# Performance work log

Measured on AMD Instinct MI355X. Metric: run time of the kernel, lower is better.

The kernel has to match this reference:

```python
import jax, jax.numpy as jnp
import numpy as np
import math

H = 512        # hidden_size (channels)
N = 64         # state_size
MAX_LEN = 4096 # kernel length L
BATCH = 8
SEQ = 4096     # seq len of input (== MAX_LEN here)


def _nplr(n):
    # HiPPO-LegS NPLR decomposition (done once at init, numpy float64 for eig stability)
    i = np.arange(n, dtype=np.float64)
    j = np.sqrt(2 * i + 1)
    A = -(np.tril(j[None, :] * j[:, None]) - np.diag(i))
    Bv = j.astype(np.complex128)
    p = j / np.sqrt(2.0)
    w, V = np.linalg.eig(A + p[None, :] * p[:, None])  # normal part; conj-pair eigvals adjacent
    w = w[::2].copy()          # [N/2]
    V = V[:, ::2].copy()       # [N, N/2]
    Bc = V.conj().T @ Bv       # [N/2]
    pc = V.conj().T @ p.astype(np.complex128)
    V_full = np.concatenate([V, V.conj()], axis=-1)      # [N, N]
    VtAV = V_full.conj().T @ A.astype(np.complex128) @ V_full  # [N, N]
    return w, pc, V, Bc, VtAV


def _ri(c):
    # complex -> trailing real/imag pair, float32 (mirrors torch.view_as_real)
    return np.stack([c.real, c.imag], axis=-1).astype(np.float32)


def setup_inputs() -> dict:
    rng = np.random.default_rng(0)
    w, p, V, Bc, Amat = _nplr(N)
    Brep = np.tile(Bc[None, :], (H, 1))                      # [H, N/2]
    C = rng.standard_normal((H, N)).astype(np.complex128)
    C = C @ V.conj()                                         # einsum('hn,nm->hm') -> [H, N/2]
    log_dt = math.log(1e-3) + (math.log(1e-1) - math.log(1e-3)) * rng.random(H)
    dt = np.exp(log_dt)[:, None, None]
    I = np.eye(N, dtype=np.complex128)[None]
    dA = np.linalg.inv(I - dt * Amat / 2) @ (I + dt * Amat / 2)   # [H, N, N]
    dA_power = I - np.linalg.matrix_power(dA, MAX_LEN)
    C2 = np.concatenate([C, C.conj()], axis=-1)              # [H, N]
    C2 = np.einsum('hmn,hm->hn', dA_power.conj(), C2)[:, : N // 2]
    p_rep = np.tile(p[None, None, :], (H, 1, 1))             # [H, 1, N/2]
    Bfull = np.concatenate([Brep[:, None, :], p_rep], axis=1)  # [H, 2, N/2]
    Cfull = np.concatenate([C2[:, None, :], p_rep], axis=1)    # [H, 2, N/2] (q == p)

    key = jax.random.key(0)
    kx, kd = jax.random.split(key)
    return {
        "x": jax.random.normal(kx, (BATCH, SEQ, H), dtype=jnp.float32),
        "log_dt": jnp.asarray(log_dt, dtype=jnp.float32),   # [H]
        "w_ri": jnp.asarray(_ri(w)),                        # [N/2, 2]
        "B_ri": jnp.asarray(_ri(Bfull)),                    # [H, 2, N/2, 2]
        "C_ri": jnp.asarray(_ri(Cfull)),                    # [H, 2, N/2, 2]
        "D": jax.random.normal(kd, (H,), dtype=jnp.float32),
    }


def _s4_kernel(log_dt, w_ri, B_ri, C_ri):
    L = MAX_LEN
    w = w_ri[..., 0] + 1j * w_ri[..., 1]   # [n] with n = N/2
    B = B_ri[..., 0] + 1j * B_ri[..., 1]   # [H, 2, n]
    C = C_ri[..., 0] + 1j * C_ri[..., 1]   # [H, 2, n]
    dt = jnp.exp(log_dt)                   # [H]
    freq = jnp.exp(-2j * jnp.pi / L * jnp.arange(L // 2 + 1))  # [F], F = L/2+1
    z = 2 * (1 - freq) / (1 + freq)        # bilinear-transformed frequencies

    v = C[:, :, None, :].conj() * B[:, None, :, :]   # [H, 2, 2, n]
    wd = w[None, :] * dt[:, None]                    # [H, n]
    # cauchy_mult: r = sum_n v/(z-w) + conj(v)/(z-conj(w)), as batched matmuls over n
    K1 = 1.0 / (z[None, None, :] - wd[:, :, None])          # [H, n, F]
    K2 = 1.0 / (z[None, None, :] - wd.conj()[:, :, None])   # [H, n, F]
    r = jnp.einsum('habn,hnf->habf', v, K1) + jnp.einsum('habn,hnf->habf', v.conj(), K2)
    r = r * dt[:, None, None, None]
    # Woodbury correction for the rank-1 (p, q) augmentation
    k_f = r[:, 0, 0, :] - r[:, 0, 1, :] * r[:, 1, 0, :] / (1 + r[:, 1, 1, :])  # [H, F]
    k_f = k_f * 2 / (1 + freq)
    return jnp.fft.irfft(k_f)   # [H, L]


def reference(x, log_dt, w_ri, B_ri, C_ri, D):
    k = _s4_kernel(log_dt, w_ri, B_ri, C_ri)     # [H, L]
    xt = jnp.transpose(x, (0, 2, 1))             # [B, H, Lx]
    L2 = 2 * MAX_LEN                              # conv pads to 2*kernel_len
    k_f = jnp.fft.rfft(k, n=L2)                  # [H, L2/2+1]
    x_f = jnp.fft.rfft(xt, n=L2)                 # [B, H, L2/2+1]
    y = jnp.fft.irfft(k_f[None] * x_f, n=L2)[..., : xt.shape[-1]]
    y = y + xt * D[None, :, None]                # skip connection
    return jnp.transpose(y, (0, 2, 1))           # [B, Lx, H]
```

## Files before the change

### kernel.cpp

```cpp
#include <hip/hip_runtime.h>
#include <math.h>

#define TPB 256
#define CTPB 512
#define KTPB 512

__device__ __forceinline__ float2 cmul(float2 a, float2 b) {
    return make_float2(a.x * b.x - a.y * b.y, a.x * b.y + a.y * b.x);
}
__device__ __forceinline__ float2 cdivf(float2 a, float2 b) {
    float inv = 1.0f / (b.x * b.x + b.y * b.y);
    return make_float2((a.x * b.x + a.y * b.y) * inv, (a.y * b.x - a.x * b.y) * inv);
}
__device__ __forceinline__ float2 cadd(float2 a, float2 b) { return make_float2(a.x + b.x, a.y + b.y); }
__device__ __forceinline__ float2 csub(float2 a, float2 b) { return make_float2(a.x - b.x, a.y - b.y); }
__device__ __forceinline__ float2 mul_i(float2 a, float d) {
    return make_float2(-d * a.y, d * a.x);
}
__device__ __forceinline__ int brev11(int x) { return (int)(__brev((unsigned)x) >> 21); }
__device__ __forceinline__ int rev8(int x) {
    return ((x & 7) << 9) | (((x >> 3) & 7) << 6) | (((x >> 6) & 7) << 3) | ((x >> 9) & 7);
}
__device__ __forceinline__ int swz(int i) { return i ^ ((i >> 4) & 15) ^ ((i >> 8) & 15); }

__device__ __forceinline__ void dft8(const float2* x, float2* y, float d) {
    const float r = 0.70710678118f;
    float2 s0 = cadd(x[0], x[4]), t0 = csub(x[0], x[4]);
    float2 s1 = cadd(x[1], x[5]), t1 = csub(x[1], x[5]);
    float2 s2 = cadd(x[2], x[6]), t2 = csub(x[2], x[6]);
    float2 s3 = cadd(x[3], x[7]), t3 = csub(x[3], x[7]);
    t1 = cmul(t1, make_float2(r, d * r));
    t2 = mul_i(t2, d);
    t3 = cmul(t3, make_float2(-r, d * r));
    float2 u0 = cadd(s0, s2), v0 = csub(s0, s2);
    float2 u1 = cadd(s1, s3), v1 = mul_i(csub(s1, s3), d);
    y[0] = cadd(u0, u1); y[4] = csub(u0, u1);
    y[2] = cadd(v0, v1); y[6] = csub(v0, v1);
    float2 p0 = cadd(t0, t2), q0 = csub(t0, t2);
    float2 p1 = cadd(t1, t3), q1 = mul_i(csub(t1, t3), d);
    y[1] = cadd(p0, p1); y[5] = csub(p0, p1);
    y[3] = cadd(q0, q1); y[7] = csub(q0, q1);
}

__device__ __forceinline__ void dft8z(float2 x0, float2 x1, float2 x2, float2 x3,
                                      float2* y, float d) {
    const float r = 0.70710678118f;
    float2 u0 = cadd(x0, x2), v0 = csub(x0, x2);
    float2 u1 = cadd(x1, x3), v1 = mul_i(csub(x1, x3), d);
    float2 t1 = cmul(x1, make_float2(r, d * r));
    float2 t2 = mul_i(x2, d);
    float2 t3 = cmul(x3, make_float2(-r, d * r));
    float2 p0 = cadd(x0, t2), q0 = csub(x0, t2);
    float2 p1 = cadd(t1, t3), q1 = mul_i(csub(t1, t3), d);
    y[0] = cadd(u0, u1); y[4] = csub(u0, u1);
    y[2] = cadd(v0, v1); y[6] = csub(v0, v1);
    y[1] = cadd(p0, p1); y[5] = csub(p0, p1);
    y[3] = cadd(q0, q1); y[7] = csub(q0, q1);
}

__device__ __forceinline__ void dft8_lo(const float2* x, float2* y, float d) {
    const float r = 0.70710678118f;
    float2 s0 = cadd(x[0], x[4]), t0 = csub(x[0], x[4]);
    float2 s1 = cadd(x[1], x[5]), t1 = csub(x[1], x[5]);
    float2 s2 = cadd(x[2], x[6]), t2 = csub(x[2], x[6]);
    float2 s3 = cadd(x[3], x[7]), t3 = csub(x[3], x[7]);
    t1 = cmul(t1, make_float2(r, d * r));
    t2 = mul_i(t2, d);
    t3 = cmul(t3, make_float2(-r, d * r));
    float2 u0 = cadd(s0, s2), v0 = csub(s0, s2);
    float2 u1 = cadd(s1, s3), v1 = mul_i(csub(s1, s3), d);
    y[0] = cadd(u0, u1);
    y[2] = cadd(v0, v1);
    float2 p0 = cadd(t0, t2), q0 = csub(t0, t2);
    float2 p1 = cadd(t1, t3), q1 = mul_i(csub(t1, t3), d);
    y[1] = cadd(p0, p1);
    y[3] = cadd(q0, q1);
}

template <int HB, int DIR>
__device__ __forceinline__ void dif_stage(float2* s, int tid) {
    __syncthreads();
    const int h = 1 << HB;
    int j = tid & (h - 1);
    int base = ((tid >> HB) << (HB + 3)) + j;
    int s0 = swz(base);
    float2 x[8];
#pragma unroll
    for (int k = 0; k < 8; ++k) x[k] = s[s0 ^ swz(k << HB)];
    float2 y[8];
    dft8(x, y, (float)DIR);
    if constexpr (HB != 0) {
        float ang = (float)DIR * 6.283185307179586f / (float)(h << 3) * (float)j;
        float c, sn;
        __sincosf(ang, &sn, &c);
        float2 w = make_float2(c, sn), wm = w;
        s[s0] = y[0];
#pragma unroll
        for (int m = 1; m < 8; ++m) {
            s[s0 ^ swz(m << HB)] = cmul(wm, y[m]);
            wm = cmul(wm, w);
        }
    } else {
#pragma unroll
        for (int m = 0; m < 8; ++m) s[s0 ^ swz(m << HB)] = y[m];
    }
}

template <int HB, int DIR>
__device__ __forceinline__ void dit_stage(float2* s, int tid) {
    __syncthreads();
    const int h = 1 << HB;
    int j = tid & (h - 1);
    int base = ((tid >> HB) << (HB + 3)) + j;
    int s0 = swz(base);
    float2 x[8];
    if constexpr (HB != 0) {
        float ang = (float)DIR * 6.283185307179586f / (float)(h << 3) * (float)j;
        float c, sn;
        __sincosf(ang, &sn, &c);
        float2 w = make_float2(c, sn);
        x[0] = s[s0];
        float2 wm = w;
#pragma unroll
        for (int k = 1; k < 8; ++k) {
            x[k] = cmul(wm, s[s0 ^ swz(k << HB)]);
            wm = cmul(wm, w);
        }
    } else {
#pragma unroll
        for (int k = 0; k < 8; ++k) x[k] = s[s0 ^ swz(k << HB)];
    }
    float2 y[8];
    dft8(x, y, (float)DIR);
#pragma unroll
    for (int m = 0; m < 8; ++m) s[s0 ^ swz(m << HB)] = y[m];
}

template <int LOGN, int NT>
__device__ void fft8_dif(float2* s, int tid, float dir) {
    const int N = 1 << LOGN;
#pragma unroll
    for (int hb = LOGN - 3; hb >= 0; hb -= 3) {
        const int h = 1 << hb;
        const float astep = dir * 6.283185307179586f / (float)(h << 3);
        __syncthreads();
#pragma unroll
        for (int it = 0; it < (N >> 3) / NT; ++it) {
            const int b = tid + it * NT;
            int j = b & (h - 1);
            int base = ((b >> hb) << (hb + 3)) + j;
            int s0 = swz(base);
            float2 x[8];
#pragma unroll
            for (int k = 0; k < 8; ++k) x[k] = s[s0 ^ swz(k << hb)];
            float2 y[8];
            dft8(x, y, dir);
            if (hb != 0) {
                float ang = astep * (float)j;
                float c, sn;
                __sincosf(ang, &sn, &c);
                float2 w = make_float2(c, sn), wm = w;
                s[s0] = y[0];
#pragma unroll
                for (int m = 1; m < 8; ++m) {
                    s[s0 ^ swz(m << hb)] = cmul(wm, y[m]);
                    wm = cmul(wm, w);
                }
            } else {
#pragma unroll
                for (int m = 0; m < 8; ++m) s[s0 ^ swz(m << hb)] = y[m];
            }
        }
    }
    __syncthreads();
}

template <int LOGN, int NT>
__device__ void fft_dif2(float2* s, int tid, float dir) {
    const int N = 1 << LOGN;
    for (int st = LOGN - 1; st >= 0; --st) {
        __syncthreads();
        int half = 1 << st;
        for (int b = tid; b < (N >> 1); b += NT) {
            int j  = b & (half - 1);
            int i0 = ((b >> st) << (st + 1)) + j;
            int i1 = i0 + half;
            float2 u = s[i0], v = s[i1];
            float2 d = make_float2(u.x - v.x, u.y - v.y);
            s[i0] = make_float2(u.x + v.x, u.y + v.y);
            if (half > 1) {
                float ang = dir * 3.14159265358979f * (float)j / (float)half;
                float c, sn;
                __sincosf(ang, &sn, &c);
                s[i1] = cmul(make_float2(c, sn), d);
            } else {
                s[i1] = d;
            }
        }
    }
    __syncthreads();
}

__global__ __launch_bounds__(TPB) void kf_kernel(
    const float* __restrict__ log_dt, const float* __restrict__ w_ri,
    const float* __restrict__ Bri, const float* __restrict__ Cri,
    float2* __restrict__ kf) {
    __shared__ float2 wds[32];
    __shared__ float aab[4][32], rab[4][32];
    __shared__ float qn[32], pn[32];
    const int h   = blockIdx.x;
    const int tid = threadIdx.x;
    const float dt = expf(log_dt[h]);
    if (tid < 32) {
        float wr = w_ri[2 * tid] * dt, wi = w_ri[2 * tid + 1] * dt;
        wds[tid] = make_float2(wr, wi);
        qn[tid]  = wr * wr + wi * wi;
        pn[tid]  = -2.0f * wr;
    }
    __syncthreads();
    if (tid < 128) {
        int a = tid >> 6, b = (tid >> 5) & 1, n = tid & 31;
        const float* Cp = Cri + (((h * 2 + a) * 32) + n) * 2;
        const float* Bp = Bri + (((h * 2 + b) * 32) + n) * 2;
        float Cr = Cp[0], Ci = Cp[1], Br = Bp[0], Bi = Bp[1];
        float2 v = make_float2(Cr * Br + Ci * Bi, Cr * Bi - Ci * Br);
        float2 wd = wds[n];
        aab[a * 2 + b][n] = -2.0f * (v.x * wd.x + v.y * wd.y);
        rab[a * 2 + b][n] = 2.0f * v.x;
    }
    __syncthreads();
    const int by   = blockIdx.y;
    const int fend = (by == 3) ? 2049 : (by + 1) * 512;
    for (int f = by * 512 + tid; f < fend; f += TPB) {
        float th = (6.283185307179586f / 4096.0f) * (float)f;
        float cf = cosf(th), sf = sinf(th);
        float2 den = make_float2(1.0f + cf, -sf);
        float zt  = 2.0f * tanf(0.5f * th);
        float zt2 = zt * zt;
        float2 r00 = make_float2(0.f, 0.f), r01 = r00, r10 = r00, r11 = r00;
        for (int n = 0; n < 32; ++n) {
            float c   = qn[n] - zt2;
            float d   = pn[n] * zt;
            float inv = 1.0f / (c * c + d * d);
            float cc = c * inv, dd = d * inv;
            float a0 = aab[0][n], b0 = rab[0][n] * zt;
            r00.x += a0 * cc + b0 * dd; r00.y += b0 * cc - a0 * dd;
            float a1 = aab[1][n], b1 = rab[1][n] * zt;
            r01.x += a1 * cc + b1 * dd; r01.y += b1 * cc - a1 * dd;
            float a2 = aab[2][n], b2 = rab[2][n] * zt;
            r10.x += a2 * cc + b2 * dd; r10.y += b2 * cc - a2 * dd;
            float a3 = aab[3][n], b3 = rab[3][n] * zt;
            r11.x += a3 * cc + b3 * dd; r11.y += b3 * cc - a3 * dd;
        }
        r00.x *= dt; r00.y *= dt; r01.x *= dt; r01.y *= dt;
        r10.x *= dt; r10.y *= dt; r11.x *= dt; r11.y *= dt;
        float2 q  = cdivf(cmul(r01, r10), make_float2(1.0f + r11.x, r11.y));
        float2 k0 = make_float2(r00.x - q.x, r00.y - q.y);
        float2 kv = cmul(k0, cdivf(make_float2(2.0f, 0.0f), den));
        kf[h * 2049 + f] = kv;
    }
}

__global__ __launch_bounds__(KTPB) void kprep_kernel(const float2* __restrict__ kf,
                                                     float2* __restrict__ Kt) {
    __shared__ float2 s[4096];
    const int hh = blockIdx.x, tid = threadIdx.x;
    const float2* X = kf + hh * 2049;
    for (int m = tid; m < 2048; m += KTPB) {
        float2 Xm = X[m];
        float2 Xc = X[2048 - m];
        if (m == 0) { Xm.y = 0.0f; Xc.y = 0.0f; }
        float2 A  = make_float2(Xm.x + Xc.x, Xm.y - Xc.y);
        float2 Bv = make_float2(Xm.x - Xc.x, Xm.y + Xc.y);
        float ang = (3.14159265358979f / 2048.0f) * (float)m;
        float c, sn;
        __sincosf(ang, &sn, &c);
        float2 O = cmul(make_float2(c, sn), Bv);
        s[m] = make_float2(0.5f * (A.x - O.y), 0.5f * (A.y + O.x));
    }
    fft_dif2<11, KTPB>(s, tid, +1.0f);
    float2 reg[4];
    const float sc = 1.0f / 2048.0f;
#pragma unroll
    for (int i = 0; i < 4; ++i) {
        int t = tid + KTPB * i;
        float2 v = s[brev11(t)];
        reg[i] = make_float2(v.x * sc, v.y * sc);
    }
    __syncthreads();
#pragma unroll
    for (int i = 0; i < 4; ++i) {
        int t = tid + KTPB * i;
        s[swz(t)]        = reg[i];
        s[swz(t + 2048)] = make_float2(0.f, 0.f);
    }
    fft8_dif<12, KTPB>(s, tid, -1.0f);
    float2* K = Kt + (size_t)hh * 4097;
    for (int p = tid; p < 4096; p += KTPB) {
        int j  = rev8(p);
        int jc = (4096 - j) & 4095;
        int pc = rev8(jc);
        float2 Yj = s[swz(p)], Yc = s[swz(pc)];
        float2 A  = make_float2(Yj.x + Yc.x, Yj.y - Yc.y);
        float2 Bv = make_float2(Yj.x - Yc.x, Yj.y + Yc.y);
        float ang = -(3.14159265358979f / 4096.0f) * (float)j;
        float c, sn;
        __sincosf(ang, &sn, &c);
        float2 t2 = cmul(make_float2(c, sn), make_float2(Bv.y, -Bv.x));
        K[p] = make_float2(0.5f * (A.x + t2.x), 0.5f * (A.y + t2.y));
        if (p == 0) K[4096] = make_float2(Yj.x - Yj.y, 0.0f);
    }
}

__global__ __launch_bounds__(TPB) void transpose_in(const float* __restrict__ x,
                                                    float* __restrict__ xt) {
    __shared__ float tile[64][65];
    const int b = blockIdx.z, t0 = blockIdx.y * 64, h0 = blockIdx.x * 64;
    const int tid = threadIdx.x;
    const float4* xv = (const float4*)(x + ((size_t)b * 4096 + t0) * 512 + h0);
#pragma unroll
    for (int i = 0; i < 4; ++i) {
        int idx = tid + TPB * i;
        int tl = idx >> 4, hq = idx & 15;
        float4 v = xv[(size_t)tl * 128 + hq];
        tile[tl][hq * 4 + 0] = v.x; tile[tl][hq * 4 + 1] = v.y;
        tile[tl][hq * 4 + 2] = v.z; tile[tl][hq * 4 + 3] = v.w;
    }
    __syncthreads();
    float* xo = xt + ((size_t)(b * 512 + h0)) * 4096 + t0;
#pragma unroll
    for (int i = 0; i < 4; ++i) {
        int idx = tid + TPB * i;
        int hl = idx >> 4, tq = idx & 15;
        float4 v = make_float4(tile[tq * 4 + 0][hl], tile[tq * 4 + 1][hl],
                               tile[tq * 4 + 2][hl], tile[tq * 4 + 3][hl]);
        ((float4*)(xo + (size_t)hl * 4096))[tq] = v;
    }
}

__global__ __launch_bounds__(CTPB) void conv_kernel(const float* xt,
                                                    const float2* __restrict__ Kt,
                                                    const float* __restrict__ Dv,
                                                    float* yt) {
    __shared__ float2 s[4096];
    const int row = blockIdx.x, tid = threadIdx.x;
    const int hch = row & 511;
    const int stid = swz(tid);
    const float2* xr = (const float2*)(xt + (size_t)row * 4096);

    {
        float2 x0 = xr[tid], x1 = xr[tid + 512], x2 = xr[tid + 1024], x3 = xr[tid + 1536];
        float2 y[8];
        dft8z(x0, x1, x2, x3, y, -1.0f);
        float ang = -(6.283185307179586f / 4096.0f) * (float)tid;
        float c, sn;
        __sincosf(ang, &sn, &c);
        float2 w = make_float2(c, sn), wm = w;
        s[stid] = y[0];
#pragma unroll
        for (int m = 1; m < 8; ++m) {
            s[stid ^ swz(m << 9)] = cmul(wm, y[m]);
            wm = cmul(wm, w);
        }
    }
    dif_stage<6, -1>(s, tid);
    dif_stage<3, -1>(s, tid);
    dif_stage<0, -1>(s, tid);
    __syncthreads();
    const float2* K = Kt + (size_t)hch * 4097;
#pragma unroll
    for (int i = 0; i < 8; ++i) {
        int p  = tid + CTPB * i;
        int sp = stid ^ swz(CTPB * i);
        if (p == 0) {
            float2 Y0 = s[sp];
            float X0 = Y0.x + Y0.y;
            float Xn = Y0.x - Y0.y;
            float Z0 = X0 * K[0].x;
            float Zn = Xn * K[4096].x;
            s[sp] = make_float2(0.5f * (Z0 + Zn), 0.5f * (Z0 - Zn));
            continue;
        }
        int j  = rev8(p);
        int jc = 4096 - j;
        int pc = rev8(jc & 4095);
        if (pc < p) continue;
        float2 Yj = s[sp], Yc = s[swz(pc)];
        float2 A  = make_float2(Yj.x + Yc.x, Yj.y - Yc.y);
        float2 Bv = make_float2(Yj.x - Yc.x, Yj.y + Yc.y);
        float ang = -(3.14159265358979f / 4096.0f) * (float)j;
        float c, sn;
        __sincosf(ang, &sn, &c);
        float2 W = make_float2(c, sn);
        float2 t2 = cmul(W, make_float2(Bv.y, -Bv.x));
        float2 Xj = make_float2(0.5f * (A.x + t2.x), 0.5f * (A.y + t2.y));
        float2 t2c = cmul(make_float2(-W.x, W.y), make_float2(Bv.y, Bv.x));
        float2 Xc2 = make_float2(0.5f * (A.x + t2c.x), 0.5f * (-A.y + t2c.y));
        float2 Zj = cmul(Xj, K[p]);
        float2 Zc = cmul(Xc2, K[pc]);
        float2 A2 = make_float2(Zj.x + Zc.x, Zj.y - Zc.y);
        float2 B2 = make_float2(Zj.x - Zc.x, Zj.y + Zc.y);
        float2 O2 = cmul(make_float2(W.x, -W.y), B2);
        s[sp] = make_float2(0.5f * (A2.x - O2.y), 0.5f * (A2.y + O2.x));
        if (pc != p) {
            float2 O2c = cmul(make_float2(-W.x, -W.y), make_float2(-B2.x, B2.y));
            s[swz(pc)] = make_float2(0.5f * (A2.x - O2c.y), 0.5f * (-A2.y + O2c.x));
        }
    }
    dit_stage<0, 1>(s, tid);
    dit_stage<3, 1>(s, tid);
    dit_stage<6, 1>(s, tid);
    __syncthreads();
    {
        float ang = (6.283185307179586f / 4096.0f) * (float)tid;
        float c, sn;
        __sincosf(ang, &sn, &c);
        float2 w = make_float2(c, sn);
        float2 x[8];
        x[0] = s[stid];
        float2 wm = w;
#pragma unroll
        for (int k = 1; k < 8; ++k) {
            x[k] = cmul(wm, s[stid ^ swz(k << 9)]);
            wm = cmul(wm, w);
        }
        float2 y[4];
        dft8_lo(x, y, 1.0f);
        const float D = Dv[hch];
        float2* yo = (float2*)(yt + (size_t)row * 4096);
        const float sc = 1.0f / 4096.0f;
#pragma unroll
        for (int m = 0; m < 4; ++m) {
            int t2 = tid + (m << 9);
            float2 xin = xr[t2];
            yo[t2] = make_float2(y[m].x * sc + D * xin.x, y[m].y * sc + D * xin.y);
        }
    }
}

__global__ __launch_bounds__(TPB) void transpose_out(const float* __restrict__ yt,
                                                     float* __restrict__ out) {
    __shared__ float tile[64][65];
    const int b = blockIdx.z, t0 = blockIdx.y * 64, h0 = blockIdx.x * 64;
    const int tid = threadIdx.x;
    const float* yp = yt + ((size_t)(b * 512 + h0)) * 4096 + t0;
#pragma unroll
    for (int i = 0; i < 4; ++i) {
        int idx = tid + TPB * i;
        int hl = idx >> 4, tq = idx & 15;
        float4 v = ((const float4*)(yp + (size_t)hl * 4096))[tq];
        tile[tq * 4 + 0][hl] = v.x; tile[tq * 4 + 1][hl] = v.y;
        tile[tq * 4 + 2][hl] = v.z; tile[tq * 4 + 3][hl] = v.w;
    }
    __syncthreads();
    float4* ov = (float4*)(out + ((size_t)b * 4096 + t0) * 512 + h0);
#pragma unroll
    for (int i = 0; i < 4; ++i) {
        int idx = tid + TPB * i;
        int tl = idx >> 4, hq = idx & 15;
        float4 v = make_float4(tile[tl][4 * hq + 0], tile[tl][4 * hq + 1],
                               tile[tl][4 * hq + 2], tile[tl][4 * hq + 3]);
        ov[(size_t)tl * 128 + hq] = v;
    }
}

extern "C" void kernel_launch(void* const* d_in, const int* in_sizes, int n_in,
                              void* d_out, int out_size, void* d_ws, size_t ws_size,
                              hipStream_t stream) {
    (void)in_sizes; (void)n_in; (void)out_size; (void)ws_size;
    const float* x      = (const float*)d_in[0];
    const float* log_dt = (const float*)d_in[1];
    const float* w_ri   = (const float*)d_in[2];
    const float* Bri    = (const float*)d_in[3];
    const float* Cri    = (const float*)d_in[4];
    const float* Dv     = (const float*)d_in[5];
    float* out = (float*)d_out;

    char* ws = (char*)d_ws;
    float*  xt = (float*)(ws);
    float2* kf = (float2*)(ws + 67108864);
    float2* Kt = (float2*)(ws + 75501568);

    kf_kernel<<<dim3(512, 4), TPB, 0, stream>>>(log_dt, w_ri, Bri, Cri, kf);
    kprep_kernel<<<512, KTPB, 0, stream>>>(kf, Kt);
    transpose_in<<<dim3(8, 64, 8), TPB, 0, stream>>>(x, xt);
    conv_kernel<<<4096, CTPB, 0, stream>>>(xt, Kt, Dv, xt);
    transpose_out<<<dim3(8, 64, 8), TPB, 0, stream>>>(xt, out);
}
```

Measured before the change: 289.2 us.

## Fold real-FFT split and kernel multiply into precomputed per-frequency P/Q coefficients

The real-to-complex untangling, kernel multiply and re-tangling in the conv kernel are replaced by one linear map per bin, z' = P*z + Q*conj(z_c). P and Q, with the 1/4096 scale folded in, are precomputed in kprep as a float4 table. The conv kernel's last DIF and first DIT radix-8 stages are fused into one register-resident dft8, multiply, idft8 block, which drops the per-bin sincos and branching. In exchange the kernel table is twice as large (float4 per bin) and kf now aliases the xt workspace, which relies on kf being consumed before transpose_in overwrites it.

```diff
diff --git a/kernel.cpp b/kernel.cpp
--- a/kernel.cpp
+++ b/kernel.cpp
@@ -262,7 +262,7 @@
 }
 
 __global__ __launch_bounds__(KTPB) void kprep_kernel(const float2* __restrict__ kf,
-                                                     float2* __restrict__ Kt) {
+                                                     float4* __restrict__ PQt) {
     __shared__ float2 s[4096];
     const int hh = blockIdx.x, tid = threadIdx.x;
     const float2* X = kf + hh * 2049;
@@ -295,20 +295,32 @@
         s[swz(t + 2048)] = make_float2(0.f, 0.f);
     }
     fft8_dif<12, KTPB>(s, tid, -1.0f);
-    float2* K = Kt + (size_t)hh * 4097;
-    for (int p = tid; p < 4096; p += KTPB) {
-        int j  = rev8(p);
-        int jc = (4096 - j) & 4095;
-        int pc = rev8(jc);
+    float4* PQ = PQt + ((size_t)hh << 12);
+    const float sc4 = 1.0f / 4096.0f;
+    const int J   = rev8(tid);
+    const int Rp  = J ? rev8(4088 - J) : 511;
+    const int pc0 = J ? rev8(4096 - J) : 0;
+#pragma unroll
+    for (int i = 0; i < 8; ++i) {
+        int p  = tid + 512 * i;
+        int pc = i ? (Rp | ((8 - i) << 9)) : pc0;
+        int j  = J | i;
         float2 Yj = s[swz(p)], Yc = s[swz(pc)];
         float2 A  = make_float2(Yj.x + Yc.x, Yj.y - Yc.y);
         float2 Bv = make_float2(Yj.x - Yc.x, Yj.y + Yc.y);
         float ang = -(3.14159265358979f / 4096.0f) * (float)j;
         float c, sn;
         __sincosf(ang, &sn, &c);
-        float2 t2 = cmul(make_float2(c, sn), make_float2(Bv.y, -Bv.x));
-        K[p] = make_float2(0.5f * (A.x + t2.x), 0.5f * (A.y + t2.y));
-        if (p == 0) K[4096] = make_float2(Yj.x - Yj.y, 0.0f);
+        float2 t2  = cmul(make_float2(c, sn), make_float2(Bv.y, -Bv.x));
+        float2 Kj  = make_float2(0.5f * (A.x + t2.x), 0.5f * (A.y + t2.y));
+        float2 t2c = cmul(make_float2(-c, sn), make_float2(Bv.y, Bv.x));
+        float2 Kc  = make_float2(0.5f * (A.x + t2c.x), 0.5f * (-A.y + t2c.y));
+        float sth = -sn, cth = c;
+        float ap = 0.5f * (1.0f - sth), bp = 0.5f * (1.0f + sth);
+        float2 P  = make_float2(ap * Kj.x + bp * Kc.x, ap * Kj.y - bp * Kc.y);
+        float2 dK = make_float2(Kj.x - Kc.x, Kj.y + Kc.y);
+        float2 Q  = make_float2(-0.5f * cth * dK.y, 0.5f * cth * dK.x);
+        PQ[p] = make_float4(P.x * sc4, P.y * sc4, Q.x * sc4, Q.y * sc4);
     }
 }
 
@@ -339,7 +351,7 @@
 }
 
 __global__ __launch_bounds__(CTPB) void conv_kernel(const float* xt,
-                                                    const float2* __restrict__ Kt,
+                                                    const float4* __restrict__ PQt,
                                                     const float* __restrict__ Dv,
                                                     float* yt) {
     __shared__ float2 s[4096];
@@ -365,49 +377,34 @@
     }
     dif_stage<6, -1>(s, tid);
     dif_stage<3, -1>(s, tid);
-    dif_stage<0, -1>(s, tid);
-    __syncthreads();
-    const float2* K = Kt + (size_t)hch * 4097;
-#pragma unroll
-    for (int i = 0; i < 8; ++i) {
-        int p  = tid + CTPB * i;
-        int sp = stid ^ swz(CTPB * i);
-        if (p == 0) {
-            float2 Y0 = s[sp];
-            float X0 = Y0.x + Y0.y;
-            float Xn = Y0.x - Y0.y;
-            float Z0 = X0 * K[0].x;
-            float Zn = Xn * K[4096].x;
-            s[sp] = make_float2(0.5f * (Z0 + Zn), 0.5f * (Z0 - Zn));
-            continue;
-        }
-        int j  = rev8(p);
-        int jc = 4096 - j;
-        int pc = rev8(jc & 4095);
-        if (pc < p) continue;
-        float2 Yj = s[sp], Yc = s[swz(pc)];
-        float2 A  = make_float2(Yj.x + Yc.x, Yj.y - Yc.y);
-        float2 Bv = make_float2(Yj.x - Yc.x, Yj.y + Yc.y);
-        float ang = -(3.14159265358979f / 4096.0f) * (float)j;
-        float c, sn;
-        __sincosf(ang, &sn, &c);
-        float2 W = make_float2(c, sn);
-        float2 t2 = cmul(W, make_float2(Bv.y, -Bv.x));
-        float2 Xj = make_float2(0.5f * (A.x + t2.x), 0.5f * (A.y + t2.y));
-        float2 t2c = cmul(make_float2(-W.x, W.y), make_float2(Bv.y, Bv.x));
-        float2 Xc2 = make_float2(0.5f * (A.x + t2c.x), 0.5f * (-A.y + t2c.y));
-        float2 Zj = cmul(Xj, K[p]);
-        float2 Zc = cmul(Xc2, K[pc]);
-        float2 A2 = make_float2(Zj.x + Zc.x, Zj.y - Zc.y);
-        float2 B2 = make_float2(Zj.x - Zc.x, Zj.y + Zc.y);
-        float2 O2 = cmul(make_float2(W.x, -W.y), B2);
-        s[sp] = make_float2(0.5f * (A2.x - O2.y), 0.5f * (A2.y + O2.x));
-        if (pc != p) {
-            float2 O2c = cmul(make_float2(-W.x, -W.y), make_float2(-B2.x, B2.y));
-            s[swz(pc)] = make_float2(0.5f * (A2.x - O2c.y), 0.5f * (-A2.y + O2c.x));
-        }
-    }
-    dit_stage<0, 1>(s, tid);
+    {
+        __syncthreads();
+        const int p0  = tid << 3;
+        const int sp0 = swz(p0);
+        float2 x[8], y[8];
+#pragma unroll
+        for (int k = 0; k < 8; ++k) x[k] = s[sp0 ^ k];
+        dft8(x, y, -1.0f);
+#pragma unroll
+        for (int k = 0; k < 8; ++k) s[sp0 ^ k] = y[k];
+        const int Jb = rev8(tid << 3);
+        const int RM = rev8(512 - Jb);
+        const float4* PQp = PQt + ((size_t)hch << 12) + p0;
+        __syncthreads();
+#pragma unroll
+        for (int k = 0; k < 8; ++k) {
+            float4 pq = PQp[k];
+            int pck = Jb ? (RM | (7 - k)) : ((8 - k) & 7);
+            float2 zc = s[swz(pck)];
+            float2 zk = y[k];
+            y[k] = make_float2(pq.x * zk.x - pq.y * zk.y + pq.z * zc.x + pq.w * zc.y,
+                               pq.x * zk.y + pq.y * zk.x + pq.w * zc.x - pq.z * zc.y);
+        }
+        __syncthreads();
+        dft8(y, x, 1.0f);
+#pragma unroll
+        for (int k = 0; k < 8; ++k) s[sp0 ^ k] = x[k];
+    }
     dit_stage<3, 1>(s, tid);
     dit_stage<6, 1>(s, tid);
     __syncthreads();
@@ -428,12 +425,11 @@
         dft8_lo(x, y, 1.0f);
         const float D = Dv[hch];
         float2* yo = (float2*)(yt + (size_t)row * 4096);
-        const float sc = 1.0f / 4096.0f;
 #pragma unroll
         for (int m = 0; m < 4; ++m) {
             int t2 = tid + (m << 9);
             float2 xin = xr[t2];
-            yo[t2] = make_float2(y[m].x * sc + D * xin.x, y[m].y * sc + D * xin.y);
+            yo[t2] = make_float2(y[m].x + D * xin.x, y[m].y + D * xin.y);
         }
     }
 }
@@ -477,13 +473,13 @@
     float* out = (float*)d_out;
 
     char* ws = (char*)d_ws;
-    float*  xt = (float*)(ws);
-    float2* kf = (float2*)(ws + 67108864);
-    float2* Kt = (float2*)(ws + 75501568);
+    float*  xt  = (float*)(ws);
+    float2* kf  = (float2*)(ws);
+    float4* PQt = (float4*)(ws + 67108864);
 
     kf_kernel<<<dim3(512, 4), TPB, 0, stream>>>(log_dt, w_ri, Bri, Cri, kf);
-    kprep_kernel<<<512, KTPB, 0, stream>>>(kf, Kt);
+    kprep_kernel<<<512, KTPB, 0, stream>>>(kf, PQt);
     transpose_in<<<dim3(8, 64, 8), TPB, 0, stream>>>(x, xt);
-    conv_kernel<<<4096, CTPB, 0, stream>>>(xt, Kt, Dv, xt);
+    conv_kernel<<<4096, CTPB, 0, stream>>>(xt, PQt, Dv, xt);
     transpose_out<<<dim3(8, 64, 8), TPB, 0, stream>>>(xt, out);
 }
```

Result: slower. 300.9 us (+4.0%).
